# Kernel tuning notes

Hardware: AMD Instinct MI355X
Metric: run time of the kernel (lower is better)

The kernel has to match this reference:

```python
import jax, jax.numpy as jnp
import numpy as np

PI = np.pi
CUTOFF = 4.0
NG = 50


def ssp(x):
    # ShiftedSoftplus: softplus(x) - log(2)
    return jax.nn.softplus(x) - jnp.asarray(np.log(2.0), x.dtype)


def setup_inputs() -> dict:
    key = jax.random.key(0)
    ks = jax.random.split(key, 16)
    N, E, H, Fc, G, L = 10000, 320000, 128, 128, 50, 6

    def rn(k, shape, s=0.05):
        return jax.random.normal(k, shape, jnp.float32) * s

    return {
        'z': jax.random.randint(ks[0], (N,), 0, 100),
        'pos': jax.random.normal(ks[1], (N, 3), jnp.float32) * 3.0,
        'edge_index': jax.random.randint(ks[2], (2, E), 0, N),
        'offset': rn(ks[3], (E, 3), 0.1),
        'cell': jnp.eye(3, dtype=jnp.float32)[None] * 10.0,
        'emb': rn(ks[4], (100, H), 1.0),
        'mlp_w1': rn(ks[5], (L, G, Fc)),
        'mlp_b1': jnp.zeros((L, Fc), jnp.float32),
        'mlp_w2': rn(ks[6], (L, Fc, Fc)),
        'mlp_b2': jnp.zeros((L, Fc), jnp.float32),
        'conv_w1': rn(ks[7], (L, H, Fc)),
        'conv_w2': rn(ks[8], (L, Fc, H)),
        'conv_b2': jnp.zeros((L, H), jnp.float32),
        'lin_w': rn(ks[9], (L, H, H)),
        'lin_b': jnp.zeros((L, H), jnp.float32),
        'out1_w': rn(ks[10], (H, H // 2)),
        'out1_b': jnp.zeros((H // 2,), jnp.float32),
        'out2_w': rn(ks[11], (H // 2, 1)),
        'out2_b': jnp.zeros((1,), jnp.float32),
    }


def _energy(pos, offset, cell, emb, mlp_w1, mlp_b1, mlp_w2, mlp_b2,
            conv_w1, conv_w2, conv_b2, lin_w, lin_b,
            out1_w, out1_b, out2_w, out2_b, z, edge_index):
    N = pos.shape[0]
    row, col = edge_index[0], edge_index[1]
    # PBC distance: d = |pos_row - pos_col + offset @ cell|
    vec = pos[row] - pos[col] + offset @ cell[0]          # [E,3]
    w = jnp.sqrt(jnp.sum(vec * vec, axis=-1))             # edge_weight [E]
    # GaussianSmearing(0, cutoff, 50)
    mu = jnp.linspace(0.0, CUTOFF, NG).astype(pos.dtype)
    coeff = -0.5 / (mu[1] - mu[0]) ** 2
    ea = jnp.exp(coeff * (w[:, None] - mu[None, :]) ** 2)  # edge_attr [E,G]
    # cosine cutoff envelope
    C = 0.5 * (jnp.cos(w * PI / CUTOFF) + 1.0)             # [E]
    h = emb[z]                                             # [N,H]
    for i in range(mlp_w1.shape[0]):
        # filter network: Linear->ssp->Linear, scaled by cosine cutoff
        W = (ssp(ea @ mlp_w1[i] + mlp_b1[i]) @ mlp_w2[i] + mlp_b2[i]) * C[:, None]  # [E,F]
        xh = h @ conv_w1[i]                                # lin1 (no bias) [N,F]
        # gather -> multiply -> scatter-add (propagate, aggr='add')
        agg = jax.ops.segment_sum(xh[row] * W, col, num_segments=N)  # [N,F]
        m = agg @ conv_w2[i] + conv_b2[i]                  # lin2 [N,H]
        h = h + (ssp(m) @ lin_w[i] + lin_b[i])             # residual InteractionBlock
    h = ssp(h @ out1_w + out1_b) @ out2_w + out2_b         # [N,1]
    return jnp.sum(h, axis=0, keepdims=True)               # readout sum, single graph -> [1,1]


def reference(z, pos, edge_index, offset, cell, emb, mlp_w1, mlp_b1, mlp_w2, mlp_b2,
              conv_w1, conv_w2, conv_b2, lin_w, lin_b, out1_w, out1_b, out2_w, out2_b):
    def e_scalar(p):
        return _energy(p, offset, cell, emb, mlp_w1, mlp_b1, mlp_w2, mlp_b2,
                       conv_w1, conv_w2, conv_b2, lin_w, lin_b,
                       out1_w, out1_b, out2_w, out2_b, z, edge_index)[0, 0]

    e, dpos = jax.value_and_grad(e_scalar)(pos)
    out = jnp.reshape(e, (1, 1))
    force = -dpos                                          # [N,3]
    return (out, force)
```

## Files before the change

kernel.cpp:

```cpp
#include <hip/hip_runtime.h>
#include <math.h>

#define LN2F 0.69314718055994530942f
#define PI_F 3.14159265358979323846f
constexpr float DMU = 4.0f/49.0f;
constexpr float GC  = -0.5f/(DMU*DMU);

typedef __bf16 bf16x8 __attribute__((ext_vector_type(8)));
typedef float  f32x4  __attribute__((ext_vector_type(4)));

__device__ __forceinline__ float sspf(float x){
  return fmaxf(x, 0.f) + log1pf(expf(-fabsf(x))) - LN2F;
}
__device__ __forceinline__ float sigf(float x){ return 1.f/(1.f+expf(-x)); }

template<int KK,int NN,bool TRB,int ATR,bool BIAS,int OTR,bool RES>
__global__ __launch_bounds__(256) void gemm_k(
    const float* __restrict__ A, int lda,
    const float* __restrict__ aux, const float* __restrict__ auxvec,
    const float* __restrict__ B, int Kreal, int Nreal,
    const float* __restrict__ bias, const float* __restrict__ res,
    const float* __restrict__ oaux, float* __restrict__ out, int M)
{
  constexpr int TM = 128, BK = 32;
  constexpr int TX = (NN==128)?16:8;
  constexpr int RT = (NN==128)?8:4;
  __shared__ float As[BK][TM+4];
  __shared__ float Bs[BK][NN+4];
  const int t = threadIdx.x;
  const int tx = t % TX, ty = t / TX;
  const int m0 = blockIdx.x * TM;
  float acc[RT][8];
  #pragma unroll
  for (int i=0;i<RT;i++)
    #pragma unroll
    for (int j=0;j<8;j++) acc[i][j]=0.f;

  for (int kc=0; kc<KK; kc+=BK){
    #pragma unroll
    for (int j=0;j<4;j++){
      int p = t + j*256;
      int m = p >> 3;
      int kv = (p & 7) << 2;
      float4 v = make_float4(0.f,0.f,0.f,0.f);
      if (m0+m < M){
        v = *(const float4*)(A + (size_t)(m0+m)*lda + kc + kv);
        if constexpr (ATR==1){ v.x=sspf(v.x); v.y=sspf(v.y); v.z=sspf(v.z); v.w=sspf(v.w); }
        else if constexpr (ATR==2){
          float4 av = *(const float4*)(aux + (size_t)(m0+m)*lda + kc + kv);
          v.x*=sigf(av.x); v.y*=sigf(av.y); v.z*=sigf(av.z); v.w*=sigf(av.w);
        }
        else if constexpr (ATR==3){
          int kg = kc+kv;
          v.x = auxvec[kg+0]*sigf(v.x); v.y = auxvec[kg+1]*sigf(v.y);
          v.z = auxvec[kg+2]*sigf(v.z); v.w = auxvec[kg+3]*sigf(v.w);
        }
      }
      As[kv+0][m]=v.x; As[kv+1][m]=v.y; As[kv+2][m]=v.z; As[kv+3][m]=v.w;
    }
    if constexpr (!TRB){
      #pragma unroll
      for (int j=0;j<(BK*NN)/1024;j++){
        int p = t + j*256;
        int k = p / (NN/4);
        int nv = (p % (NN/4)) << 2;
        float4 v = make_float4(0.f,0.f,0.f,0.f);
        if (kc + k < Kreal) v = *(const float4*)(B + (size_t)(kc+k)*NN + nv);
        *(float4*)&Bs[k][nv] = v;
      }
    } else {
      #pragma unroll
      for (int j=0;j<(BK*NN)/1024;j++){
        int p = t + j*256;
        int n = p >> 3;
        int kv = (p & 7) << 2;
        float4 v = make_float4(0.f,0.f,0.f,0.f);
        if (n < Nreal) v = *(const float4*)(B + (size_t)n*KK + kc + kv);
        Bs[kv+0][n]=v.x; Bs[kv+1][n]=v.y; Bs[kv+2][n]=v.z; Bs[kv+3][n]=v.w;
      }
    }
    __syncthreads();
    #pragma unroll
    for (int k=0;k<BK;k++){
      float a[RT], b[8];
      #pragma unroll
      for (int i=0;i<RT;i+=4) *(float4*)&a[i] = *(const float4*)&As[k][ty*RT+i];
      *(float4*)&b[0] = *(const float4*)&Bs[k][tx*8];
      *(float4*)&b[4] = *(const float4*)&Bs[k][tx*8+4];
      #pragma unroll
      for (int i=0;i<RT;i++)
        #pragma unroll
        for (int j=0;j<8;j++)
          acc[i][j] = fmaf(a[i], b[j], acc[i][j]);
    }
    __syncthreads();
  }
  #pragma unroll
  for (int i=0;i<RT;i++){
    int r = m0 + ty*RT + i;
    if (r < M){
      float vo[8];
      #pragma unroll
      for (int j=0;j<8;j++){
        float v = acc[i][j];
        int c = tx*8 + j;
        if constexpr (BIAS) v += bias[c];
        if constexpr (OTR==1) v = sspf(v);
        else if constexpr (OTR==2) v *= sigf(oaux[(size_t)r*NN + c]);
        if constexpr (RES) v += res[(size_t)r*NN + c];
        vo[j] = v;
      }
      *(float4*)(out + (size_t)r*NN + tx*8)     = make_float4(vo[0],vo[1],vo[2],vo[3]);
      *(float4*)(out + (size_t)r*NN + tx*8 + 4) = make_float4(vo[4],vo[5],vo[6],vo[7]);
    }
  }
}

__global__ __launch_bounds__(256) void fwd_edge_k(
    const float* __restrict__ wv, const float* __restrict__ Cv,
    const int* __restrict__ ei, int E,
    const __bf16* __restrict__ W1t, const float* __restrict__ b1,
    const __bf16* __restrict__ W2t, const float* __restrict__ b2,
    const float* __restrict__ xh, float* __restrict__ agg)
{
  __shared__ __align__(16) __bf16 W2s[128][136];
  __shared__ __align__(16) __bf16 s1t[64][136];
  __shared__ float wrow[64], Ce[64];
  __shared__ int rowi[64], coli[64];
  const int t = threadIdx.x;
  const int e0 = blockIdx.x*64;

  #pragma unroll
  for (int it=0; it<8; ++it){
    int p = t + it*256;
    int row = p >> 4;
    int ko = (p & 15)*8;
    *(uint4*)&W2s[row][ko] = *(const uint4*)(W2t + (size_t)row*128 + ko);
  }
  if (t < 64){
    int e = e0 + t;
    bool ok = e < E;
    wrow[t] = ok ? wv[e] : 0.f;
    Ce[t]   = ok ? Cv[e] : 0.f;
    rowi[t] = ok ? ei[e] : 0;
    coli[t] = ok ? ei[E+e] : 0;
  }
  __syncthreads();

  const int wid = t>>6, lane = t&63, quad = lane>>4, ln = lane&15;
  f32x4 acc[8];
  #pragma unroll
  for (int nt=0;nt<8;nt++) acc[nt] = (f32x4){0.f,0.f,0.f,0.f};

  const float wa = wrow[wid*16 + ln];
  #pragma unroll
  for (int ks=0; ks<64; ks+=32){
    bf16x8 a;
    #pragma unroll
    for (int j=0;j<8;j++){
      int k = ks + quad*8 + j;
      float d = wa - (float)k*DMU;
      a[j] = (k<50) ? (__bf16)__expf(GC*d*d) : (__bf16)0.f;
    }
    #pragma unroll
    for (int nt=0; nt<8; nt++){
      bf16x8 b = *(const bf16x8*)(W1t + (size_t)(nt*16+ln)*64 + ks + quad*8);
      acc[nt] = __builtin_amdgcn_mfma_f32_16x16x32_bf16(a, b, acc[nt], 0, 0, 0);
    }
  }
  #pragma unroll
  for (int nt=0; nt<8; nt++){
    int c = nt*16 + ln;
    float bb = b1[c];
    #pragma unroll
    for (int reg=0; reg<4; reg++){
      int r = wid*16 + quad*4 + reg;
      s1t[r][c] = (__bf16)sspf(acc[nt][reg] + bb);
    }
  }
  __syncthreads();

  #pragma unroll
  for (int nt=0;nt<8;nt++) acc[nt] = (f32x4){0.f,0.f,0.f,0.f};
  #pragma unroll
  for (int ks=0; ks<128; ks+=32){
    bf16x8 a = *(const bf16x8*)&s1t[wid*16 + ln][ks + quad*8];
    #pragma unroll
    for (int nt=0; nt<8; nt++){
      bf16x8 b = *(const bf16x8*)&W2s[nt*16 + ln][ks + quad*8];
      acc[nt] = __builtin_amdgcn_mfma_f32_16x16x32_bf16(a, b, acc[nt], 0, 0, 0);
    }
  }

  #pragma unroll
  for (int reg=0; reg<4; reg++){
    int r = wid*16 + quad*4 + reg;
    int e = e0 + r;
    if (e < E){
      float ce = Ce[r];
      size_t ri = (size_t)rowi[r]*128;
      size_t ci = (size_t)coli[r]*128;
      #pragma unroll
      for (int nt=0; nt<8; nt++){
        int c = nt*16 + ln;
        float wf = acc[nt][reg] + b2[c];
        atomicAdd(&agg[ci + c], xh[ri + c]*ce*wf);
      }
    }
  }
}

__global__ __launch_bounds__(256) void bwd_edge_k(
    const float* __restrict__ wv, const float* __restrict__ Cv,
    const int* __restrict__ ei, int E,
    const __bf16* __restrict__ W1t, const float* __restrict__ b1,
    const __bf16* __restrict__ W2t, const float* __restrict__ b2,
    const __bf16* __restrict__ W2c, const __bf16* __restrict__ W1c,
    const float* __restrict__ dagg, const float* __restrict__ xh,
    float* __restrict__ dxh, float* __restrict__ dC, float* __restrict__ dw,
    int accum)
{
  __shared__ __align__(16) __bf16 Ws[128][136];
  __shared__ __align__(16) __bf16 tb[64][136];
  __shared__ float wrow[64], Ce[64];
  __shared__ int rowi[64], coli[64];
  const int t = threadIdx.x;
  const int e0 = blockIdx.x*64;

  #pragma unroll
  for (int it=0; it<8; ++it){
    int p = t + it*256;
    int row = p >> 4;
    int ko = (p & 15)*8;
    *(uint4*)&Ws[row][ko] = *(const uint4*)(W2t + (size_t)row*128 + ko);
  }
  if (t < 64){
    int e = e0 + t;
    bool ok = e < E;
    wrow[t] = ok ? wv[e] : 0.f;
    Ce[t]   = ok ? Cv[e] : 0.f;
    rowi[t] = ok ? ei[e] : 0;
    coli[t] = ok ? ei[E+e] : 0;
  }
  __syncthreads();

  const int wid = t>>6, lane = t&63, quad = lane>>4, ln = lane&15;
  f32x4 acc[8];
  float sig[8][4];
  #pragma unroll
  for (int nt=0;nt<8;nt++) acc[nt] = (f32x4){0.f,0.f,0.f,0.f};

  const float wa = wrow[wid*16 + ln];
  #pragma unroll
  for (int ks=0; ks<64; ks+=32){
    bf16x8 a;
    #pragma unroll
    for (int j=0;j<8;j++){
      int k = ks + quad*8 + j;
      float d = wa - (float)k*DMU;
      a[j] = (k<50) ? (__bf16)__expf(GC*d*d) : (__bf16)0.f;
    }
    #pragma unroll
    for (int nt=0; nt<8; nt++){
      bf16x8 b = *(const bf16x8*)(W1t + (size_t)(nt*16+ln)*64 + ks + quad*8);
      acc[nt] = __builtin_amdgcn_mfma_f32_16x16x32_bf16(a, b, acc[nt], 0, 0, 0);
    }
  }
  #pragma unroll
  for (int nt=0; nt<8; nt++){
    int c = nt*16 + ln;
    float bb = b1[c];
    #pragma unroll
    for (int reg=0; reg<4; reg++){
      int r = wid*16 + quad*4 + reg;
      float t1 = acc[nt][reg] + bb;
      sig[nt][reg] = sigf(t1);
      tb[r][c] = (__bf16)sspf(t1);
    }
  }
  __syncthreads();

  #pragma unroll
  for (int nt=0;nt<8;nt++) acc[nt] = (f32x4){0.f,0.f,0.f,0.f};
  #pragma unroll
  for (int ks=0; ks<128; ks+=32){
    bf16x8 a = *(const bf16x8*)&tb[wid*16 + ln][ks + quad*8];
    #pragma unroll
    for (int nt=0; nt<8; nt++){
      bf16x8 b = *(const bf16x8*)&Ws[nt*16 + ln][ks + quad*8];
      acc[nt] = __builtin_amdgcn_mfma_f32_16x16x32_bf16(a, b, acc[nt], 0, 0, 0);
    }
  }
  __syncthreads();

  #pragma unroll
  for (int reg=0; reg<4; reg++){
    int r = wid*16 + quad*4 + reg;
    int e = e0 + r;
    float dcp = 0.f;
    if (e < E){
      float ce = Ce[r];
      size_t ri = (size_t)rowi[r]*128;
      size_t ci = (size_t)coli[r]*128;
      #pragma unroll
      for (int nt=0; nt<8; nt++){
        int c = nt*16 + ln;
        float wf = acc[nt][reg] + b2[c];
        float da = dagg[ci + c];
        float xv = xh[ri + c];
        dcp += da*xv*wf;
        atomicAdd(&dxh[ri + c], da*ce*wf);
        tb[r][c] = (__bf16)(da*xv*ce);
      }
    } else {
      #pragma unroll
      for (int nt=0; nt<8; nt++) tb[r][nt*16+ln] = (__bf16)0.f;
    }
    dcp += __shfl_xor(dcp, 1);
    dcp += __shfl_xor(dcp, 2);
    dcp += __shfl_xor(dcp, 4);
    dcp += __shfl_xor(dcp, 8);
    if (ln==0 && e < E) dC[e] = accum ? (dC[e]+dcp) : dcp;
  }
  #pragma unroll
  for (int it=0; it<8; ++it){
    int p = t + it*256;
    int row = p >> 4;
    int ko = (p & 15)*8;
    *(uint4*)&Ws[row][ko] = *(const uint4*)(W2c + (size_t)row*128 + ko);
  }
  __syncthreads();

  #pragma unroll
  for (int nt=0;nt<8;nt++) acc[nt] = (f32x4){0.f,0.f,0.f,0.f};
  #pragma unroll
  for (int ks=0; ks<128; ks+=32){
    bf16x8 a = *(const bf16x8*)&tb[wid*16 + ln][ks + quad*8];
    #pragma unroll
    for (int nt=0; nt<8; nt++){
      bf16x8 b = *(const bf16x8*)&Ws[nt*16 + ln][ks + quad*8];
      acc[nt] = __builtin_amdgcn_mfma_f32_16x16x32_bf16(a, b, acc[nt], 0, 0, 0);
    }
  }
  __syncthreads();
  #pragma unroll
  for (int nt=0; nt<8; nt++){
    int c = nt*16 + ln;
    #pragma unroll
    for (int reg=0; reg<4; reg++){
      int r = wid*16 + quad*4 + reg;
      tb[r][c] = (__bf16)(acc[nt][reg] * sig[nt][reg]);
    }
  }
  __syncthreads();

  #pragma unroll
  for (int nt=0;nt<4;nt++) acc[nt] = (f32x4){0.f,0.f,0.f,0.f};
  #pragma unroll
  for (int ks=0; ks<128; ks+=32){
    bf16x8 a = *(const bf16x8*)&tb[wid*16 + ln][ks + quad*8];
    #pragma unroll
    for (int nt=0; nt<4; nt++){
      bf16x8 b = *(const bf16x8*)(W1c + (size_t)(nt*16+ln)*128 + ks + quad*8);
      acc[nt] = __builtin_amdgcn_mfma_f32_16x16x32_bf16(a, b, acc[nt], 0, 0, 0);
    }
  }
  #pragma unroll
  for (int reg=0; reg<4; reg++){
    int r = wid*16 + quad*4 + reg;
    int e = e0 + r;
    float w = wrow[r];
    float s = 0.f;
    #pragma unroll
    for (int nt=0; nt<4; nt++){
      int c = nt*16 + ln;
      if (c < 50){
        float d = w - (float)c*DMU;
        s += acc[nt][reg] * (2.f*GC*d) * __expf(GC*d*d);
      }
    }
    s += __shfl_xor(s, 1);
    s += __shfl_xor(s, 2);
    s += __shfl_xor(s, 4);
    s += __shfl_xor(s, 8);
    if (ln==0 && e < E) dw[e] = accum ? (dw[e]+s) : s;
  }
}

__global__ void convw_k(const float* __restrict__ w1, const float* __restrict__ w2,
                        __bf16* __restrict__ W1t, __bf16* __restrict__ W2t,
                        __bf16* __restrict__ W2c, __bf16* __restrict__ W1c, int total)
{
  int idx = blockIdx.x*256 + threadIdx.x;
  if (idx >= total) return;
  int l = idx / 49152;
  int r = idx % 49152;
  if (r < 8192){
    int n = r / 64, k = r % 64;
    float v = (k<50) ? w1[(size_t)l*6400 + k*128 + n] : 0.f;
    W1t[(size_t)l*8192 + r] = (__bf16)v;
  } else if (r < 24576){
    int r2 = r - 8192;
    int n = r2 / 128, k = r2 % 128;
    W2t[(size_t)l*16384 + r2] = (__bf16)w2[(size_t)l*16384 + k*128 + n];
  } else if (r < 40960){
    int r2 = r - 24576;
    W2c[(size_t)l*16384 + r2] = (__bf16)w2[(size_t)l*16384 + r2];
  } else {
    int r2 = r - 40960;
    int n = r2 / 128, k = r2 % 128;
    float v = (n<50) ? w1[(size_t)l*6400 + n*128 + k] : 0.f;
    W1c[(size_t)l*8192 + r2] = (__bf16)v;
  }
}

__global__ void edge_geom_k(const float* __restrict__ pos, const int* __restrict__ ei,
                            const float* __restrict__ off, const float* __restrict__ cell,
                            float* __restrict__ wv, float* __restrict__ Cv, int E)
{
  int e = blockIdx.x*256 + threadIdx.x;
  if (e>=E) return;
  int r = ei[e], c = ei[E+e];
  float o0=off[3*e], o1=off[3*e+1], o2=off[3*e+2];
  float d0 = o0*cell[0] + o1*cell[3] + o2*cell[6];
  float d1 = o0*cell[1] + o1*cell[4] + o2*cell[7];
  float d2 = o0*cell[2] + o1*cell[5] + o2*cell[8];
  float v0 = pos[3*r+0]-pos[3*c+0]+d0;
  float v1 = pos[3*r+1]-pos[3*c+1]+d1;
  float v2 = pos[3*r+2]-pos[3*c+2]+d2;
  float w = sqrtf(v0*v0+v1*v1+v2*v2);
  wv[e]=w;
  Cv[e]=0.5f*cosf(w*(PI_F/4.0f)) + 0.5f;
}

__global__ void embed_k(const float* __restrict__ emb, const int* __restrict__ z,
                        float* __restrict__ h, int total){
  int i = blockIdx.x*256 + threadIdx.x;
  if (i < total){ int n=i>>7, j=i&127; h[i] = emb[(size_t)z[n]*128 + j]; }
}

__global__ void head_k(const float* __restrict__ u, const float* __restrict__ o2,
                       const float* __restrict__ o2b, float* __restrict__ out0, int N){
  int n = blockIdx.x*256 + threadIdx.x;
  float s = 0.f;
  if (n < N){
    #pragma unroll
    for (int k=0;k<64;k+=4){
      float4 uv = *(const float4*)(u + (size_t)n*64 + k);
      float4 ov = *(const float4*)(o2 + k);
      s += sspf(uv.x)*ov.x + sspf(uv.y)*ov.y + sspf(uv.z)*ov.z + sspf(uv.w)*ov.w;
    }
  }
  #pragma unroll
  for (int m=1;m<64;m<<=1) s += __shfl_xor(s, m);
  __shared__ float red[4];
  int lane = threadIdx.x&63, w = threadIdx.x>>6;
  if (lane==0) red[w]=s;
  __syncthreads();
  if (threadIdx.x==0){
    float tot = red[0]+red[1]+red[2]+red[3];
    if (blockIdx.x==0) tot += (float)N * o2b[0];
    atomicAdd(out0, tot);
  }
}

__global__ void force_k(const float* __restrict__ dw, const float* __restrict__ dC,
                        const float* __restrict__ wv,
                        const float* __restrict__ pos, const int* __restrict__ ei,
                        const float* __restrict__ off, const float* __restrict__ cell,
                        float* __restrict__ f, int E)
{
  int e = blockIdx.x*256 + threadIdx.x;
  if (e>=E) return;
  int r = ei[e], c = ei[E+e];
  float o0=off[3*e], o1=off[3*e+1], o2=off[3*e+2];
  float d0 = o0*cell[0] + o1*cell[3] + o2*cell[6];
  float d1 = o0*cell[1] + o1*cell[4] + o2*cell[7];
  float d2 = o0*cell[2] + o1*cell[5] + o2*cell[8];
  float v0 = pos[3*r+0]-pos[3*c+0]+d0;
  float v1 = pos[3*r+1]-pos[3*c+1]+d1;
  float v2 = pos[3*r+2]-pos[3*c+2]+d2;
  float w = wv[e];
  float dwt = dw[e] + dC[e] * (-0.5f*(PI_F/4.0f)) * sinf(w*(PI_F/4.0f));
  float s = dwt / w;
  atomicAdd(&f[3*r+0], -v0*s); atomicAdd(&f[3*r+1], -v1*s); atomicAdd(&f[3*r+2], -v2*s);
  atomicAdd(&f[3*c+0],  v0*s); atomicAdd(&f[3*c+1],  v1*s); atomicAdd(&f[3*c+2],  v2*s);
}

extern "C" void kernel_launch(void* const* d_in, const int* in_sizes, int n_in,
                              void* d_out, int out_size, void* d_ws, size_t ws_size,
                              hipStream_t stream)
{
  const int N = in_sizes[0];
  const int E = in_sizes[2]/2;
  const int L = 6;
  const int* z        = (const int*)d_in[0];
  const float* pos    = (const float*)d_in[1];
  const int* ei       = (const int*)d_in[2];
  const float* offset = (const float*)d_in[3];
  const float* cell   = (const float*)d_in[4];
  const float* emb    = (const float*)d_in[5];
  const float* mlp_w1 = (const float*)d_in[6];
  const float* mlp_b1 = (const float*)d_in[7];
  const float* mlp_w2 = (const float*)d_in[8];
  const float* mlp_b2 = (const float*)d_in[9];
  const float* conv_w1= (const float*)d_in[10];
  const float* conv_w2= (const float*)d_in[11];
  const float* conv_b2= (const float*)d_in[12];
  const float* lin_w  = (const float*)d_in[13];
  const float* lin_b  = (const float*)d_in[14];
  const float* out1_w = (const float*)d_in[15];
  const float* out1_b = (const float*)d_in[16];
  const float* out2_w = (const float*)d_in[17];
  const float* out2_b = (const float*)d_in[18];
  float* out = (float*)d_out;

  char* wp = (char*)d_ws;
  auto alloc = [&](size_t bytes)->char*{ char* p = wp; wp += (bytes + 255) & ~(size_t)255; return p; };
  float* wbuf = (float*)alloc((size_t)E*4);
  float* Cbuf = (float*)alloc((size_t)E*4);
  float* dCb  = (float*)alloc((size_t)E*4);
  float* dwb  = (float*)alloc((size_t)E*4);
  float* xh   = (float*)alloc((size_t)L*N*128*4);
  float* mbuf = (float*)alloc((size_t)L*N*128*4);
  float* ubuf = (float*)alloc((size_t)N*64*4);
  float* hbuf = (float*)alloc((size_t)N*128*4);
  float* Gbuf = (float*)alloc((size_t)N*128*4);
  float* bufA = (float*)alloc((size_t)N*128*4);
  float* bufB = (float*)alloc((size_t)N*128*4);
  float* bufC = (float*)alloc((size_t)N*128*4);
  float* aggb = (float*)alloc((size_t)N*128*4);
  __bf16* W1t = (__bf16*)alloc((size_t)L*8192*2);
  __bf16* W2t = (__bf16*)alloc((size_t)L*16384*2);
  __bf16* W2c = (__bf16*)alloc((size_t)L*16384*2);
  __bf16* W1c = (__bf16*)alloc((size_t)L*8192*2);

  const int egrid = (E+255)/256;
  const int eg64 = (E+63)/64;
  const int ng = (N+127)/128;
  const int wtotal = L*49152;

  hipMemsetAsync(d_out, 0, (size_t)out_size*4, stream);
  convw_k<<<(wtotal+255)/256,256,0,stream>>>(mlp_w1, mlp_w2, W1t, W2t, W2c, W1c, wtotal);
  edge_geom_k<<<egrid,256,0,stream>>>(pos, ei, offset, cell, wbuf, Cbuf, E);
  embed_k<<<(N*128+255)/256,256,0,stream>>>(emb, z, hbuf, N*128);

  for (int i=0;i<L;i++){
    const float* b1i = mlp_b1 + (size_t)i*128;
    const float* b2i = mlp_b2 + (size_t)i*128;
    const float* cw1i= conv_w1+ (size_t)i*128*128;
    const float* cw2i= conv_w2+ (size_t)i*128*128;
    const float* cb2i= conv_b2+ (size_t)i*128;
    const float* lwi = lin_w  + (size_t)i*128*128;
    const float* lbi = lin_b  + (size_t)i*128;
    float* xhi = xh   + (size_t)i*N*128;
    float* mi  = mbuf + (size_t)i*N*128;

    gemm_k<128,128,false,0,false,0,false><<<ng,256,0,stream>>>(
      hbuf, 128, nullptr, nullptr, cw1i, 128, 128, nullptr, nullptr, nullptr, xhi, N);
    hipMemsetAsync(aggb, 0, (size_t)N*128*4, stream);
    fwd_edge_k<<<eg64,256,0,stream>>>(
      wbuf, Cbuf, ei, E, W1t + (size_t)i*8192, b1i, W2t + (size_t)i*16384, b2i, xhi, aggb);
    gemm_k<128,128,false,0,true,0,false><<<ng,256,0,stream>>>(
      aggb, 128, nullptr, nullptr, cw2i, 128, 128, cb2i, nullptr, nullptr, mi, N);
    gemm_k<128,128,false,1,true,0,true><<<ng,256,0,stream>>>(
      mi, 128, nullptr, nullptr, lwi, 128, 128, lbi, hbuf, nullptr, hbuf, N);
  }

  gemm_k<128,64,false,0,true,0,false><<<ng,256,0,stream>>>(
    hbuf, 128, nullptr, nullptr, out1_w, 128, 64, out1_b, nullptr, nullptr, ubuf, N);
  head_k<<<(N+255)/256,256,0,stream>>>(ubuf, out2_w, out2_b, out, N);
  gemm_k<64,128,true,3,false,0,false><<<ng,256,0,stream>>>(
    ubuf, 64, nullptr, out2_w, out1_w, 64, 128, nullptr, nullptr, nullptr, Gbuf, N);

  for (int i=L-1;i>=0;i--){
    const float* b1i = mlp_b1 + (size_t)i*128;
    const float* b2i = mlp_b2 + (size_t)i*128;
    const float* cw1i= conv_w1+ (size_t)i*128*128;
    const float* cw2i= conv_w2+ (size_t)i*128*128;
    const float* lwi = lin_w  + (size_t)i*128*128;
    float* xhi = xh   + (size_t)i*N*128;
    float* mi  = mbuf + (size_t)i*N*128;
    int first = (i==L-1) ? 0 : 1;

    gemm_k<128,128,true,0,false,0,false><<<ng,256,0,stream>>>(
      Gbuf, 128, nullptr, nullptr, lwi, 128, 128, nullptr, nullptr, nullptr, bufA, N);
    gemm_k<128,128,true,2,false,0,false><<<ng,256,0,stream>>>(
      bufA, 128, mi, nullptr, cw2i, 128, 128, nullptr, nullptr, nullptr, bufB, N);
    hipMemsetAsync(bufC, 0, (size_t)N*128*4, stream);
    bwd_edge_k<<<eg64,256,0,stream>>>(
      wbuf, Cbuf, ei, E,
      W1t + (size_t)i*8192, b1i, W2t + (size_t)i*16384, b2i,
      W2c + (size_t)i*16384, W1c + (size_t)i*8192,
      bufB, xhi, bufC, dCb, dwb, first);
    gemm_k<128,128,true,0,false,0,true><<<ng,256,0,stream>>>(
      bufC, 128, nullptr, nullptr, cw1i, 128, 128, nullptr, Gbuf, nullptr, Gbuf, N);
  }

  force_k<<<egrid,256,0,stream>>>(dwb, dCb, wbuf, pos, ei, offset, cell, out+1, E);
}
```

Baseline: 4.447 ms.

## Read edge-MLP weights from global/L2 instead of LDS and use fast math intrinsics

Drops the per-block staging of the 128x128 bf16 W2 and W2c matrices into shared memory in the forward and backward edge kernels. The MFMA B operands are now read straight from global memory, so LDS use shrinks, occupancy can rise, and launch_bounds now request 4 blocks per CU. Softplus, sigmoid and the cutoff sine switch to fast hardware intrinsics (__expf, __logf, rcp, __sinf). The cost is repeated global/L2 reads of the weights inside the MFMA loop and slightly lower numerical accuracy.

```diff
diff --git a/kernel.cpp b/kernel.cpp
--- a/kernel.cpp
+++ b/kernel.cpp
@@ -10,9 +10,11 @@
 typedef float  f32x4  __attribute__((ext_vector_type(4)));
 
 __device__ __forceinline__ float sspf(float x){
-  return fmaxf(x, 0.f) + log1pf(expf(-fabsf(x))) - LN2F;
-}
-__device__ __forceinline__ float sigf(float x){ return 1.f/(1.f+expf(-x)); }
+  return fmaxf(x, 0.f) + __logf(1.f + __expf(-fabsf(x))) - LN2F;
+}
+__device__ __forceinline__ float sigf(float x){
+  return __builtin_amdgcn_rcpf(1.f + __expf(-x));
+}
 
 template<int KK,int NN,bool TRB,int ATR,bool BIAS,int OTR,bool RES>
 __global__ __launch_bounds__(256) void gemm_k(
@@ -116,27 +118,19 @@
   }
 }
 
-__global__ __launch_bounds__(256) void fwd_edge_k(
+__global__ __launch_bounds__(256,4) void fwd_edge_k(
     const float* __restrict__ wv, const float* __restrict__ Cv,
     const int* __restrict__ ei, int E,
     const __bf16* __restrict__ W1t, const float* __restrict__ b1,
     const __bf16* __restrict__ W2t, const float* __restrict__ b2,
     const float* __restrict__ xh, float* __restrict__ agg)
 {
-  __shared__ __align__(16) __bf16 W2s[128][136];
   __shared__ __align__(16) __bf16 s1t[64][136];
   __shared__ float wrow[64], Ce[64];
   __shared__ int rowi[64], coli[64];
   const int t = threadIdx.x;
   const int e0 = blockIdx.x*64;
 
-  #pragma unroll
-  for (int it=0; it<8; ++it){
-    int p = t + it*256;
-    int row = p >> 4;
-    int ko = (p & 15)*8;
-    *(uint4*)&W2s[row][ko] = *(const uint4*)(W2t + (size_t)row*128 + ko);
-  }
   if (t < 64){
     int e = e0 + t;
     bool ok = e < E;
@@ -187,7 +181,7 @@
     bf16x8 a = *(const bf16x8*)&s1t[wid*16 + ln][ks + quad*8];
     #pragma unroll
     for (int nt=0; nt<8; nt++){
-      bf16x8 b = *(const bf16x8*)&W2s[nt*16 + ln][ks + quad*8];
+      bf16x8 b = *(const bf16x8*)(W2t + (size_t)(nt*16+ln)*128 + ks + quad*8);
       acc[nt] = __builtin_amdgcn_mfma_f32_16x16x32_bf16(a, b, acc[nt], 0, 0, 0);
     }
   }
@@ -210,7 +204,7 @@
   }
 }
 
-__global__ __launch_bounds__(256) void bwd_edge_k(
+__global__ __launch_bounds__(256,4) void bwd_edge_k(
     const float* __restrict__ wv, const float* __restrict__ Cv,
     const int* __restrict__ ei, int E,
     const __bf16* __restrict__ W1t, const float* __restrict__ b1,
@@ -220,20 +214,12 @@
     float* __restrict__ dxh, float* __restrict__ dC, float* __restrict__ dw,
     int accum)
 {
-  __shared__ __align__(16) __bf16 Ws[128][136];
   __shared__ __align__(16) __bf16 tb[64][136];
   __shared__ float wrow[64], Ce[64];
   __shared__ int rowi[64], coli[64];
   const int t = threadIdx.x;
   const int e0 = blockIdx.x*64;
 
-  #pragma unroll
-  for (int it=0; it<8; ++it){
-    int p = t + it*256;
-    int row = p >> 4;
-    int ko = (p & 15)*8;
-    *(uint4*)&Ws[row][ko] = *(const uint4*)(W2t + (size_t)row*128 + ko);
-  }
   if (t < 64){
     int e = e0 + t;
     bool ok = e < E;
@@ -287,7 +273,7 @@
     bf16x8 a = *(const bf16x8*)&tb[wid*16 + ln][ks + quad*8];
     #pragma unroll
     for (int nt=0; nt<8; nt++){
-      bf16x8 b = *(const bf16x8*)&Ws[nt*16 + ln][ks + quad*8];
+      bf16x8 b = *(const bf16x8*)(W2t + (size_t)(nt*16+ln)*128 + ks + quad*8);
       acc[nt] = __builtin_amdgcn_mfma_f32_16x16x32_bf16(a, b, acc[nt], 0, 0, 0);
     }
   }
@@ -322,13 +308,6 @@
     dcp += __shfl_xor(dcp, 8);
     if (ln==0 && e < E) dC[e] = accum ? (dC[e]+dcp) : dcp;
   }
-  #pragma unroll
-  for (int it=0; it<8; ++it){
-    int p = t + it*256;
-    int row = p >> 4;
-    int ko = (p & 15)*8;
-    *(uint4*)&Ws[row][ko] = *(const uint4*)(W2c + (size_t)row*128 + ko);
-  }
   __syncthreads();
 
   #pragma unroll
@@ -338,7 +317,7 @@
     bf16x8 a = *(const bf16x8*)&tb[wid*16 + ln][ks + quad*8];
     #pragma unroll
     for (int nt=0; nt<8; nt++){
-      bf16x8 b = *(const bf16x8*)&Ws[nt*16 + ln][ks + quad*8];
+      bf16x8 b = *(const bf16x8*)(W2c + (size_t)(nt*16+ln)*128 + ks + quad*8);
       acc[nt] = __builtin_amdgcn_mfma_f32_16x16x32_bf16(a, b, acc[nt], 0, 0, 0);
     }
   }
@@ -481,7 +460,7 @@
   float v1 = pos[3*r+1]-pos[3*c+1]+d1;
   float v2 = pos[3*r+2]-pos[3*c+2]+d2;
   float w = wv[e];
-  float dwt = dw[e] + dC[e] * (-0.5f*(PI_F/4.0f)) * sinf(w*(PI_F/4.0f));
+  float dwt = dw[e] + dC[e] * (-0.5f*(PI_F/4.0f)) * __sinf(w*(PI_F/4.0f));
   float s = dwt / w;
   atomicAdd(&f[3*r+0], -v0*s); atomicAdd(&f[3*r+1], -v1*s); atomicAdd(&f[3*r+2], -v2*s);
   atomicAdd(&f[3*c+0],  v0*s); atomicAdd(&f[3*c+1],  v1*s); atomicAdd(&f[3*c+2],  v2*s);
```

Result: slower. 5.009 ms (+12.6%).
